# Kernel tuning notes

Measured on AMD Instinct MI355X. Metric: run time of the kernel, lower is better.

Reference implementation:

```python
import jax, jax.numpy as jnp
import numpy as np

B, T = 1024, 128
F_DIM, Z_DIM, TXT_DIM, H = 1024, 256, 768, 8
EPS = 1e-5


def layer_norm(x, g, b):
    mu = jnp.mean(x, axis=-1, keepdims=True)
    var = jnp.var(x, axis=-1, keepdims=True)
    return (x - mu) * jax.lax.rsqrt(var + EPS) * g + b


def setup_inputs() -> dict:
    key = jax.random.key(0)
    ks = jax.random.split(key, 16)
    s = lambda fi, fo: 1.0 / np.sqrt(fi)  # rough init scale
    inp = {
        "x": jax.random.normal(ks[0], (B, F_DIM), jnp.float32),
        "z": jax.random.normal(ks[1], (B, Z_DIM), jnp.float32),
        "text_feat": jax.random.normal(ks[2], (B, T, TXT_DIM), jnp.float32),
        "attention": jnp.ones((B, T), jnp.int32),
        # FiLM
        "Wg": jax.random.normal(ks[3], (F_DIM, Z_DIM), jnp.float32) * s(Z_DIM, F_DIM),
        "bg": jnp.zeros((F_DIM,), jnp.float32),
        "Wb": jax.random.normal(ks[4], (F_DIM, Z_DIM), jnp.float32) * s(Z_DIM, F_DIM),
        "bb": jnp.zeros((F_DIM,), jnp.float32),
        # Linear block (linear -> LayerNorm)
        "Wl": jax.random.normal(ks[5], (F_DIM, F_DIM), jnp.float32) * s(F_DIM, F_DIM),
        "bl": jnp.zeros((F_DIM,), jnp.float32),
        "ln1_g": jnp.ones((F_DIM,), jnp.float32),
        "ln1_b": jnp.zeros((F_DIM,), jnp.float32),
        # cross attention projections
        "Wq": jax.random.normal(ks[6], (F_DIM, F_DIM), jnp.float32) * s(F_DIM, F_DIM),
        "bq": jnp.zeros((F_DIM,), jnp.float32),
        "Wk": jax.random.normal(ks[7], (F_DIM, TXT_DIM), jnp.float32) * s(TXT_DIM, F_DIM),
        "bk": jnp.zeros((F_DIM,), jnp.float32),
        "Wv": jax.random.normal(ks[8], (F_DIM, TXT_DIM), jnp.float32) * s(TXT_DIM, F_DIM),
        "bv": jnp.zeros((F_DIM,), jnp.float32),
        "Wo": jax.random.normal(ks[9], (F_DIM, F_DIM), jnp.float32) * s(F_DIM, F_DIM),
        "bo": jnp.zeros((F_DIM,), jnp.float32),
        # post-attention LayerNorm
        "ln2_g": jnp.ones((F_DIM,), jnp.float32),
        "ln2_b": jnp.zeros((F_DIM,), jnp.float32),
    }
    return inp


def reference(x, z, text_feat, attention, Wg, bg, Wb, bb, Wl, bl, ln1_g, ln1_b,
              Wq, bq, Wk, bk, Wv, bv, Wo, bo, ln2_g, ln2_b):
    d = F_DIM // H
    # FiLM params from condition z
    gamma = z @ Wg.T + bg            # [B, F]
    beta = z @ Wb.T + bb             # [B, F]
    # Linear block: linear -> LayerNorm (dropout p=0, identity activation)
    out = layer_norm(x @ Wl.T + bl, ln1_g, ln1_b)
    out = out * (1.0 + gamma) + beta  # FiLM modulation
    # single-query multi-head cross attention
    q = (out @ Wq.T + bq).reshape(B, H, d)                 # [B, H, d] (query len 1)
    k = (text_feat @ Wk.T + bk).reshape(B, T, H, d)         # [B, T, H, d]
    v = (text_feat @ Wv.T + bv).reshape(B, T, H, d)
    scores = jnp.einsum("bhd,bthd->bht", q, k) / jnp.sqrt(jnp.float32(d))  # [B, H, T]
    mask = (attention[:, None, :] != 0)                     # [B, 1, T]
    scores = jnp.where(mask, scores, -jnp.inf)
    attn = jax.nn.softmax(scores, axis=-1)                  # [B, H, T]
    ctx = jnp.einsum("bht,bthd->bhd", attn, v).reshape(B, F_DIM)
    attn_out = ctx @ Wo.T + bo
    out = out + layer_norm(attn_out, ln2_g, ln2_b)
    return jax.nn.gelu(out, approximate=False)
```

## Files before the change

kernel.cpp:

```cpp
#include <hip/hip_runtime.h>

#define EPS 1e-5f

typedef __bf16 bf16x8 __attribute__((ext_vector_type(8)));
typedef float f32x4 __attribute__((ext_vector_type(4)));
typedef ushort ushort8 __attribute__((ext_vector_type(8)));

static __device__ __forceinline__ ushort f2bf(float x) {
    union { float f; unsigned u; } v; v.f = x;
    unsigned r = v.u + 0x7fffu + ((v.u >> 16) & 1u);
    return (ushort)(r >> 16);
}
static __device__ __forceinline__ float bf2f(ushort u) {
    union { unsigned u32; float f; } v; v.u32 = (unsigned)u << 16;
    return v.f;
}

__global__ __launch_bounds__(256)
void gemm_nt_mfma(const float* __restrict__ A, int lda, int Aoffz,
                  const ushort* __restrict__ W, int ldw, int Woffz,
                  float* __restrict__ C, int ldc, int Coffz,
                  const float* __restrict__ bias, int boffz,
                  float scale, int K)
{
    const int z = blockIdx.z;
    A += (size_t)z * Aoffz;
    W += (size_t)z * Woffz;
    C += (size_t)z * Coffz;
    const int bm = blockIdx.y * 64, bn = blockIdx.x * 64;

    __shared__ ushort As[64][72];
    __shared__ ushort Bs[64][72];

    const int tid  = threadIdx.x;
    const int lane = tid & 63, wv = tid >> 6;
    const int wm = (wv >> 1) * 32, wn = (wv & 1) * 32;

    const int srow = tid >> 2;
    const int scol = (tid & 3) * 16;
    const float*  Agp = A + (size_t)(bm + srow) * lda + scol;
    const ushort* Wgp = W + (size_t)(bn + srow) * ldw + scol;

    const int fr = lane & 15, fk = (lane >> 4) * 8;

    f32x4 acc[2][2] = {};

    for (int kt = 0; kt < K; kt += 64) {
        f32x4 a0 = *(const f32x4*)(Agp + kt + 0);
        f32x4 a1 = *(const f32x4*)(Agp + kt + 4);
        f32x4 a2 = *(const f32x4*)(Agp + kt + 8);
        f32x4 a3 = *(const f32x4*)(Agp + kt + 12);
        ushort8 b0 = *(const ushort8*)(Wgp + kt);
        ushort8 b1 = *(const ushort8*)(Wgp + kt + 8);

        ushort8 u0, u1;
        u0[0]=f2bf(a0[0]); u0[1]=f2bf(a0[1]); u0[2]=f2bf(a0[2]); u0[3]=f2bf(a0[3]);
        u0[4]=f2bf(a1[0]); u0[5]=f2bf(a1[1]); u0[6]=f2bf(a1[2]); u0[7]=f2bf(a1[3]);
        u1[0]=f2bf(a2[0]); u1[1]=f2bf(a2[1]); u1[2]=f2bf(a2[2]); u1[3]=f2bf(a2[3]);
        u1[4]=f2bf(a3[0]); u1[5]=f2bf(a3[1]); u1[6]=f2bf(a3[2]); u1[7]=f2bf(a3[3]);

        *(ushort8*)&As[srow][scol]     = u0;
        *(ushort8*)&As[srow][scol + 8] = u1;
        *(ushort8*)&Bs[srow][scol]     = b0;
        *(ushort8*)&Bs[srow][scol + 8] = b1;
        __syncthreads();

        #pragma unroll
        for (int ks = 0; ks < 64; ks += 32) {
            bf16x8 af0 = *(const bf16x8*)&As[wm + fr][ks + fk];
            bf16x8 af1 = *(const bf16x8*)&As[wm + 16 + fr][ks + fk];
            bf16x8 bf0 = *(const bf16x8*)&Bs[wn + fr][ks + fk];
            bf16x8 bf1 = *(const bf16x8*)&Bs[wn + 16 + fr][ks + fk];
            acc[0][0] = __builtin_amdgcn_mfma_f32_16x16x32_bf16(af0, bf0, acc[0][0], 0, 0, 0);
            acc[0][1] = __builtin_amdgcn_mfma_f32_16x16x32_bf16(af0, bf1, acc[0][1], 0, 0, 0);
            acc[1][0] = __builtin_amdgcn_mfma_f32_16x16x32_bf16(af1, bf0, acc[1][0], 0, 0, 0);
            acc[1][1] = __builtin_amdgcn_mfma_f32_16x16x32_bf16(af1, bf1, acc[1][1], 0, 0, 0);
        }
        __syncthreads();
    }

    const int rbase = (lane >> 4) * 4;
    #pragma unroll
    for (int mi = 0; mi < 2; ++mi) {
        #pragma unroll
        for (int ni = 0; ni < 2; ++ni) {
            const int col = bn + wn + ni * 16 + fr;
            const float bvv = bias ? (bias + (size_t)z * boffz)[col] : 0.f;
            #pragma unroll
            for (int r = 0; r < 4; ++r) {
                const int row = bm + wm + mi * 16 + rbase + r;
                C[(size_t)row * ldc + col] = acc[mi][ni][r] * scale + bvv;
            }
        }
    }
}

__global__ __launch_bounds__(256)
void cvt_all(const float* __restrict__ Wl, const float* __restrict__ Wq,
             const float* __restrict__ Wo, const float* __restrict__ Wv,
             const float* __restrict__ Wg, const float* __restrict__ Wb,
             const float* __restrict__ bg, const float* __restrict__ bb,
             ushort* __restrict__ WlB, ushort* __restrict__ WqB,
             ushort* __restrict__ WoB, ushort* __restrict__ WvB,
             ushort* __restrict__ WgbB, float* __restrict__ bgb)
{
    int gid = blockIdx.x * 256 + threadIdx.x;
    if (gid < 512) {
        f32x4 v = (gid < 256) ? *(const f32x4*)(bg + gid * 4)
                              : *(const f32x4*)(bb + (gid - 256) * 4);
        *(f32x4*)(bgb + gid * 4) = v;
    }
    const float* src; ushort* dst; int off;
    if      (gid <  262144) { src = Wl; dst = WlB;           off = gid;          }
    else if (gid <  524288) { src = Wq; dst = WqB;           off = gid - 262144; }
    else if (gid <  786432) { src = Wo; dst = WoB;           off = gid - 524288; }
    else if (gid <  983040) { src = Wv; dst = WvB;           off = gid - 786432; }
    else if (gid < 1048576) { src = Wg; dst = WgbB;          off = gid - 983040; }
    else if (gid < 1114112) { src = Wb; dst = WgbB + 262144; off = gid - 1048576;}
    else return;
    f32x4 v = *(const f32x4*)(src + (size_t)off * 4);
    ushort4 o;
    o.x = f2bf(v[0]); o.y = f2bf(v[1]); o.z = f2bf(v[2]); o.w = f2bf(v[3]);
    *(ushort4*)(dst + (size_t)off * 4) = o;
}

__global__ __launch_bounds__(256)
void transpose_wk(const float* __restrict__ Wk, ushort* __restrict__ WkT)
{
    __shared__ ushort s[32][33];
    const int h  = blockIdx.z;
    const int c0 = blockIdx.x * 32, d0 = blockIdx.y * 32;
    const int tx = threadIdx.x & 31, ty = threadIdx.x >> 5;
    #pragma unroll
    for (int i = 0; i < 4; ++i) {
        int d = d0 + ty + i * 8;
        s[ty + i * 8][tx] = f2bf(Wk[(size_t)(h * 128 + d) * 768 + c0 + tx]);
    }
    __syncthreads();
    #pragma unroll
    for (int i = 0; i < 4; ++i) {
        int c = c0 + ty + i * 8;
        WkT[((size_t)h * 768 + c) * 128 + d0 + tx] = s[tx][ty + i * 8];
    }
}

__device__ inline void block_reduce2(float& a, float& b, float* sred)
{
    #pragma unroll
    for (int off = 32; off; off >>= 1) {
        a += __shfl_xor(a, off);
        b += __shfl_xor(b, off);
    }
    int w = threadIdx.x >> 6, lane = threadIdx.x & 63;
    if (lane == 0) { sred[w * 2] = a; sred[w * 2 + 1] = b; }
    __syncthreads();
    a = sred[0] + sred[2] + sred[4] + sred[6];
    b = sred[1] + sred[3] + sred[5] + sred[7];
}

__global__ __launch_bounds__(256)
void rowops1(const float* __restrict__ h1, const float* __restrict__ gb,
             const float* __restrict__ g, const float* __restrict__ bta,
             float* __restrict__ out)
{
    __shared__ float sred[8];
    int b = blockIdx.x, tid = threadIdx.x;
    const float4 v = ((const float4*)(h1 + (size_t)b * 1024))[tid];
    float s  = v.x + v.y + v.z + v.w;
    float ss = v.x * v.x + v.y * v.y + v.z * v.z + v.w * v.w;
    block_reduce2(s, ss, sred);
    float mu  = s * (1.f / 1024.f);
    float var = ss * (1.f / 1024.f) - mu * mu;
    float rs  = rsqrtf(var + EPS);
    float4 gv = ((const float4*)g)[tid];
    float4 bv = ((const float4*)bta)[tid];
    float4 ga = ((const float4*)(gb + (size_t)b * 2048))[tid];
    float4 be = ((const float4*)(gb + (size_t)b * 2048 + 1024))[tid];
    float4 o;
    o.x = ((v.x - mu) * rs * gv.x + bv.x) * (1.f + ga.x) + be.x;
    o.y = ((v.y - mu) * rs * gv.y + bv.y) * (1.f + ga.y) + be.y;
    o.z = ((v.z - mu) * rs * gv.z + bv.z) * (1.f + ga.z) + be.z;
    o.w = ((v.w - mu) * rs * gv.w + bv.w) * (1.f + ga.w) + be.w;
    ((float4*)(out + (size_t)b * 1024))[tid] = o;
}

__global__ __launch_bounds__(256)
void rowops2(const float* __restrict__ outp, const float* __restrict__ ao,
             const float* __restrict__ g, const float* __restrict__ bta,
             float* __restrict__ dst)
{
    __shared__ float sred[8];
    int b = blockIdx.x, tid = threadIdx.x;
    const float4 v = ((const float4*)(ao + (size_t)b * 1024))[tid];
    float s  = v.x + v.y + v.z + v.w;
    float ss = v.x * v.x + v.y * v.y + v.z * v.z + v.w * v.w;
    block_reduce2(s, ss, sred);
    float mu  = s * (1.f / 1024.f);
    float var = ss * (1.f / 1024.f) - mu * mu;
    float rs  = rsqrtf(var + EPS);
    float4 gv = ((const float4*)g)[tid];
    float4 bv = ((const float4*)bta)[tid];
    float4 ov = ((const float4*)(outp + (size_t)b * 1024))[tid];
    float y0 = ov.x + ((v.x - mu) * rs * gv.x + bv.x);
    float y1 = ov.y + ((v.y - mu) * rs * gv.y + bv.y);
    float y2 = ov.z + ((v.z - mu) * rs * gv.z + bv.z);
    float y3 = ov.w + ((v.w - mu) * rs * gv.w + bv.w);
    float4 o;
    o.x = 0.5f * y0 * (1.f + erff(y0 * 0.70710678118654752f));
    o.y = 0.5f * y1 * (1.f + erff(y1 * 0.70710678118654752f));
    o.z = 0.5f * y2 * (1.f + erff(y2 * 0.70710678118654752f));
    o.w = 0.5f * y3 * (1.f + erff(y3 * 0.70710678118654752f));
    ((float4*)(dst + (size_t)b * 1024))[tid] = o;
}

__global__ __launch_bounds__(256)
void attn_fused(const float* __restrict__ tf, const float* __restrict__ qt,
                const int* __restrict__ att, float* __restrict__ ctxtf)
{
    const int b = blockIdx.x;
    const int tid = threadIdx.x, lane = tid & 63, wv = tid >> 6;

    __shared__ ushort qtS[16][776];
    __shared__ ushort TF[32][776];
    __shared__ float s_sc[8][32];
    __shared__ float ps[8][32];

    const float* tfb = tf + (size_t)b * 98304;
    const float* qtb = qt + (size_t)b * 6144;

    {
        const int r  = tid >> 5;
        const int c0 = (tid & 31) * 24;
        #pragma unroll
        for (int j = 0; j < 6; ++j) {
            f32x4 v = *(const f32x4*)&qtb[r * 768 + c0 + 4 * j];
            ushort4 o;
            o.x = f2bf(v[0]); o.y = f2bf(v[1]); o.z = f2bf(v[2]); o.w = f2bf(v[3]);
            *(ushort4*)&qtS[r][c0 + 4 * j] = o;
        }
        const ushort4 z4 = {0, 0, 0, 0};
        #pragma unroll
        for (int j = 0; j < 6; ++j)
            *(ushort4*)&qtS[8 + r][c0 + 4 * j] = z4;
    }

    float acc[2][3][4] = {};
    float mrun = -INFINITY, srun = 0.f;
    const int fr = lane & 15, fko = (lane >> 4) * 8;
    const int hloc = lane >> 5, tl = lane & 31;
    const int h_own = 2 * wv + hloc;
    const int h0 = 2 * wv;

    for (int s = 0; s < 4; ++s) {
        __syncthreads();
        {
            const int r  = tid >> 3;
            const int c0 = (tid & 7) * 96;
            const float* srcr = tfb + (size_t)(s * 32 + r) * 768 + c0;
            #pragma unroll
            for (int j = 0; j < 24; ++j) {
                f32x4 v = *(const f32x4*)(srcr + 4 * j);
                ushort4 o;
                o.x = f2bf(v[0]); o.y = f2bf(v[1]); o.z = f2bf(v[2]); o.w = f2bf(v[3]);
                *(ushort4*)&TF[r][c0 + 4 * j] = o;
            }
        }
        __syncthreads();
        if (wv < 2) {
            f32x4 sacc = {0.f, 0.f, 0.f, 0.f};
            #pragma unroll
            for (int ks = 0; ks < 768; ks += 32) {
                bf16x8 aq = *(const bf16x8*)&qtS[fr][ks + fko];
                bf16x8 bt = *(const bf16x8*)&TF[wv * 16 + fr][ks + fko];
                sacc = __builtin_amdgcn_mfma_f32_16x16x32_bf16(aq, bt, sacc, 0, 0, 0);
            }
            if (lane < 32) {
                const int hbase = (lane >> 4) * 4;
                #pragma unroll
                for (int r = 0; r < 4; ++r)
                    s_sc[hbase + r][wv * 16 + (lane & 15)] = sacc[r];
            }
        }
        __syncthreads();
        {
            const int mask = att[b * 128 + s * 32 + tl];
            float sv = mask ? s_sc[h_own][tl] : -INFINITY;
            float mx = sv;
            mx = fmaxf(mx, __shfl_xor(mx, 16));
            mx = fmaxf(mx, __shfl_xor(mx, 8));
            mx = fmaxf(mx, __shfl_xor(mx, 4));
            mx = fmaxf(mx, __shfl_xor(mx, 2));
            mx = fmaxf(mx, __shfl_xor(mx, 1));
            float mnew = fmaxf(mrun, mx);
            float p = mask ? __expf(sv - mnew) : 0.f;
            float f = (mnew == -INFINITY) ? 1.f : __expf(mrun - mnew);
            float psum = p;
            psum += __shfl_xor(psum, 16);
            psum += __shfl_xor(psum, 8);
            psum += __shfl_xor(psum, 4);
            psum += __shfl_xor(psum, 2);
            psum += __shfl_xor(psum, 1);
            srun = srun * f + psum;
            mrun = mnew;
            ps[h_own][tl] = p;
            const float f0 = __shfl(f, 0);
            const float f1 = __shfl(f, 32);
            #pragma unroll
            for (int k = 0; k < 3; ++k)
                #pragma unroll
                for (int e = 0; e < 4; ++e) {
                    acc[0][k][e] *= f0;
                    acc[1][k][e] *= f1;
                }
        }
        {
            #pragma unroll 8
            for (int t = 0; t < 32; ++t) {
                const float p0 = ps[h0][t];
                const float p1 = ps[h0 + 1][t];
                #pragma unroll
                for (int k = 0; k < 3; ++k) {
                    ushort4 u = *(const ushort4*)&TF[t][4 * lane + 256 * k];
                    float x0 = bf2f(u.x), x1 = bf2f(u.y), x2 = bf2f(u.z), x3 = bf2f(u.w);
                    acc[0][k][0] += p0 * x0; acc[0][k][1] += p0 * x1;
                    acc[0][k][2] += p0 * x2; acc[0][k][3] += p0 * x3;
                    acc[1][k][0] += p1 * x0; acc[1][k][1] += p1 * x1;
                    acc[1][k][2] += p1 * x2; acc[1][k][3] += p1 * x3;
                }
            }
        }
    }

    const float sum0 = __shfl(srun, 0);
    const float sum1 = __shfl(srun, 32);
    const float i0 = 1.f / sum0, i1 = 1.f / sum1;
    #pragma unroll
    for (int k = 0; k < 3; ++k) {
        f32x4 o0, o1;
        #pragma unroll
        for (int e = 0; e < 4; ++e) {
            o0[e] = acc[0][k][e] * i0;
            o1[e] = acc[1][k][e] * i1;
        }
        *(f32x4*)&ctxtf[(size_t)b * 6144 + (size_t)h0 * 768 + 4 * lane + 256 * k] = o0;
        *(f32x4*)&ctxtf[(size_t)b * 6144 + (size_t)(h0 + 1) * 768 + 4 * lane + 256 * k] = o1;
    }
}

extern "C" void kernel_launch(void* const* d_in, const int* in_sizes, int n_in,
                              void* d_out, int out_size, void* d_ws, size_t ws_size,
                              hipStream_t stream)
{
    const float* x    = (const float*)d_in[0];
    const float* zc   = (const float*)d_in[1];
    const float* tf   = (const float*)d_in[2];
    const int*   att  = (const int*)d_in[3];
    const float* Wg   = (const float*)d_in[4];
    const float* bg   = (const float*)d_in[5];
    const float* Wb   = (const float*)d_in[6];
    const float* bb   = (const float*)d_in[7];
    const float* Wl   = (const float*)d_in[8];
    const float* bl   = (const float*)d_in[9];
    const float* ln1g = (const float*)d_in[10];
    const float* ln1b = (const float*)d_in[11];
    const float* Wq   = (const float*)d_in[12];
    const float* bq   = (const float*)d_in[13];
    const float* Wk   = (const float*)d_in[14];
    const float* Wv   = (const float*)d_in[16];
    const float* bv   = (const float*)d_in[17];
    const float* Wo   = (const float*)d_in[18];
    const float* bo   = (const float*)d_in[19];
    const float* ln2g = (const float*)d_in[20];
    const float* ln2b = (const float*)d_in[21];

    float* ws = (float*)d_ws;
    const size_t M1 = 1u << 20;
    float* OUT   = ws;
    float* H1    = ws + 1 * M1;
    float* GB    = ws + 2 * M1;
    float* Q     = ws + 4 * M1;
    float* QT    = ws + 5 * M1;
    float* CTXTF = ws + 11 * M1;
    float* AO    = ws + 17 * M1;
    float* bgb   = ws + 18 * M1;
    float* CTX   = H1;

    ushort* wb16 = (ushort*)(ws + 19 * M1);
    ushort* WlB  = wb16;
    ushort* WqB  = wb16 + 1 * M1;
    ushort* WoB  = wb16 + 2 * M1;
    ushort* WvB  = wb16 + 3 * M1;
    ushort* WgbB = wb16 + 3 * M1 + 786432;
    ushort* WkT  = wb16 + 3 * M1 + 786432 + 524288;

    dim3 blk(256);

    cvt_all<<<dim3(4352), blk, 0, stream>>>(Wl, Wq, Wo, Wv, Wg, Wb, bg, bb,
                                            WlB, WqB, WoB, WvB, WgbB, bgb);
    transpose_wk<<<dim3(24, 4, 8), blk, 0, stream>>>(Wk, WkT);

    gemm_nt_mfma<<<dim3(16, 16, 1), blk, 0, stream>>>(x, 1024, 0, WlB, 1024, 0,
        H1, 1024, 0, bl, 0, 1.f, 1024);
    gemm_nt_mfma<<<dim3(32, 16, 1), blk, 0, stream>>>(zc, 256, 0, WgbB, 256, 0,
        GB, 2048, 0, bgb, 0, 1.f, 256);
    rowops1<<<dim3(1024), blk, 0, stream>>>(H1, GB, ln1g, ln1b, OUT);
    gemm_nt_mfma<<<dim3(16, 16, 1), blk, 0, stream>>>(OUT, 1024, 0, WqB, 1024, 0,
        Q, 1024, 0, bq, 0, 1.f, 1024);
    gemm_nt_mfma<<<dim3(12, 16, 8), blk, 0, stream>>>(Q, 1024, 128, WkT, 128, 98304,
        QT, 6144, 768, nullptr, 0, 0.08838834764831845f, 128);
    attn_fused<<<dim3(1024), blk, 0, stream>>>(tf, QT, att, CTXTF);
    gemm_nt_mfma<<<dim3(2, 16, 8), blk, 0, stream>>>(CTXTF, 6144, 768, WvB, 768, 98304,
        CTX, 1024, 128, bv, 128, 1.f, 768);
    gemm_nt_mfma<<<dim3(16, 16, 1), blk, 0, stream>>>(CTX, 1024, 0, WoB, 1024, 0,
        AO, 1024, 0, bo, 0, 1.f, 1024);
    rowops2<<<dim3(1024), blk, 0, stream>>>(OUT, AO, ln2g, ln2b, (float*)d_out);
}
```

Measured before the change: 709.0 us.

## Store intermediates in bf16 and prefetch next K tile in GEMM

```diff
diff --git a/kernel.cpp b/kernel.cpp
--- a/kernel.cpp
+++ b/kernel.cpp
@@ -16,17 +16,17 @@
     return v.f;
 }
 
-__global__ __launch_bounds__(256)
-void gemm_nt_mfma(const float* __restrict__ A, int lda, int Aoffz,
-                  const ushort* __restrict__ W, int ldw, int Woffz,
-                  float* __restrict__ C, int ldc, int Coffz,
-                  const float* __restrict__ bias, int boffz,
-                  float scale, int K)
+template<int OB>
+__global__ __launch_bounds__(256)
+void gemm_bb(const ushort* __restrict__ A, int lda, int Aoffz,
+             const ushort* __restrict__ W, int ldw, int Woffz,
+             void* __restrict__ Cv, int ldc, int Coffz,
+             const float* __restrict__ bias, int boffz,
+             float scale, int K)
 {
     const int z = blockIdx.z;
     A += (size_t)z * Aoffz;
     W += (size_t)z * Woffz;
-    C += (size_t)z * Coffz;
     const int bm = blockIdx.y * 64, bn = blockIdx.x * 64;
 
     __shared__ ushort As[64][72];
@@ -38,33 +38,30 @@
 
     const int srow = tid >> 2;
     const int scol = (tid & 3) * 16;
-    const float*  Agp = A + (size_t)(bm + srow) * lda + scol;
+    const ushort* Agp = A + (size_t)(bm + srow) * lda + scol;
     const ushort* Wgp = W + (size_t)(bn + srow) * ldw + scol;
 
     const int fr = lane & 15, fk = (lane >> 4) * 8;
 
     f32x4 acc[2][2] = {};
 
+    ushort8 a0 = *(const ushort8*)(Agp);
+    ushort8 a1 = *(const ushort8*)(Agp + 8);
+    ushort8 b0 = *(const ushort8*)(Wgp);
+    ushort8 b1 = *(const ushort8*)(Wgp + 8);
+
     for (int kt = 0; kt < K; kt += 64) {
-        f32x4 a0 = *(const f32x4*)(Agp + kt + 0);
-        f32x4 a1 = *(const f32x4*)(Agp + kt + 4);
-        f32x4 a2 = *(const f32x4*)(Agp + kt + 8);
-        f32x4 a3 = *(const f32x4*)(Agp + kt + 12);
-        ushort8 b0 = *(const ushort8*)(Wgp + kt);
-        ushort8 b1 = *(const ushort8*)(Wgp + kt + 8);
-
-        ushort8 u0, u1;
-        u0[0]=f2bf(a0[0]); u0[1]=f2bf(a0[1]); u0[2]=f2bf(a0[2]); u0[3]=f2bf(a0[3]);
-        u0[4]=f2bf(a1[0]); u0[5]=f2bf(a1[1]); u0[6]=f2bf(a1[2]); u0[7]=f2bf(a1[3]);
-        u1[0]=f2bf(a2[0]); u1[1]=f2bf(a2[1]); u1[2]=f2bf(a2[2]); u1[3]=f2bf(a2[3]);
-        u1[4]=f2bf(a3[0]); u1[5]=f2bf(a3[1]); u1[6]=f2bf(a3[2]); u1[7]=f2bf(a3[3]);
-
-        *(ushort8*)&As[srow][scol]     = u0;
-        *(ushort8*)&As[srow][scol + 8] = u1;
+        *(ushort8*)&As[srow][scol]     = a0;
+        *(ushort8*)&As[srow][scol + 8] = a1;
         *(ushort8*)&Bs[srow][scol]     = b0;
         *(ushort8*)&Bs[srow][scol + 8] = b1;
         __syncthreads();
-
+        if (kt + 64 < K) {
+            a0 = *(const ushort8*)(Agp + kt + 64);
+            a1 = *(const ushort8*)(Agp + kt + 64 + 8);
+            b0 = *(const ushort8*)(Wgp + kt + 64);
+            b1 = *(const ushort8*)(Wgp + kt + 64 + 8);
+        }
         #pragma unroll
         for (int ks = 0; ks < 64; ks += 32) {
             bf16x8 af0 = *(const bf16x8*)&As[wm + fr][ks + fk];
@@ -89,7 +86,12 @@
             #pragma unroll
             for (int r = 0; r < 4; ++r) {
                 const int row = bm + wm + mi * 16 + rbase + r;
-                C[(size_t)row * ldc + col] = acc[mi][ni][r] * scale + bvv;
+                const float val = acc[mi][ni][r] * scale + bvv;
+                if (OB) {
+                    ((ushort*)Cv)[(size_t)z * Coffz + (size_t)row * ldc + col] = f2bf(val);
+                } else {
+                    ((float*)Cv)[(size_t)z * Coffz + (size_t)row * ldc + col] = val;
+                }
             }
         }
     }
@@ -99,10 +101,12 @@
 void cvt_all(const float* __restrict__ Wl, const float* __restrict__ Wq,
              const float* __restrict__ Wo, const float* __restrict__ Wv,
              const float* __restrict__ Wg, const float* __restrict__ Wb,
+             const float* __restrict__ x,  const float* __restrict__ zc,
              const float* __restrict__ bg, const float* __restrict__ bb,
              ushort* __restrict__ WlB, ushort* __restrict__ WqB,
              ushort* __restrict__ WoB, ushort* __restrict__ WvB,
-             ushort* __restrict__ WgbB, float* __restrict__ bgb)
+             ushort* __restrict__ WgbB, ushort* __restrict__ xB,
+             ushort* __restrict__ zB, float* __restrict__ bgb)
 {
     int gid = blockIdx.x * 256 + threadIdx.x;
     if (gid < 512) {
@@ -117,6 +121,8 @@
     else if (gid <  983040) { src = Wv; dst = WvB;           off = gid - 786432; }
     else if (gid < 1048576) { src = Wg; dst = WgbB;          off = gid - 983040; }
     else if (gid < 1114112) { src = Wb; dst = WgbB + 262144; off = gid - 1048576;}
+    else if (gid < 1376256) { src = x;  dst = xB;            off = gid - 1114112;}
+    else if (gid < 1441792) { src = zc; dst = zB;            off = gid - 1376256;}
     else return;
     f32x4 v = *(const f32x4*)(src + (size_t)off * 4);
     ushort4 o;
@@ -161,7 +167,7 @@
 __global__ __launch_bounds__(256)
 void rowops1(const float* __restrict__ h1, const float* __restrict__ gb,
              const float* __restrict__ g, const float* __restrict__ bta,
-             float* __restrict__ out)
+             ushort* __restrict__ outb)
 {
     __shared__ float sred[8];
     int b = blockIdx.x, tid = threadIdx.x;
@@ -176,16 +182,16 @@
     float4 bv = ((const float4*)bta)[tid];
     float4 ga = ((const float4*)(gb + (size_t)b * 2048))[tid];
     float4 be = ((const float4*)(gb + (size_t)b * 2048 + 1024))[tid];
-    float4 o;
-    o.x = ((v.x - mu) * rs * gv.x + bv.x) * (1.f + ga.x) + be.x;
-    o.y = ((v.y - mu) * rs * gv.y + bv.y) * (1.f + ga.y) + be.y;
-    o.z = ((v.z - mu) * rs * gv.z + bv.z) * (1.f + ga.z) + be.z;
-    o.w = ((v.w - mu) * rs * gv.w + bv.w) * (1.f + ga.w) + be.w;
-    ((float4*)(out + (size_t)b * 1024))[tid] = o;
-}
-
-__global__ __launch_bounds__(256)
-void rowops2(const float* __restrict__ outp, const float* __restrict__ ao,
+    ushort4 o;
+    o.x = f2bf(((v.x - mu) * rs * gv.x + bv.x) * (1.f + ga.x) + be.x);
+    o.y = f2bf(((v.y - mu) * rs * gv.y + bv.y) * (1.f + ga.y) + be.y);
+    o.z = f2bf(((v.z - mu) * rs * gv.z + bv.z) * (1.f + ga.z) + be.z);
+    o.w = f2bf(((v.w - mu) * rs * gv.w + bv.w) * (1.f + ga.w) + be.w);
+    ((ushort4*)(outb + (size_t)b * 1024))[tid] = o;
+}
+
+__global__ __launch_bounds__(256)
+void rowops2(const ushort* __restrict__ outb, const float* __restrict__ ao,
              const float* __restrict__ g, const float* __restrict__ bta,
              float* __restrict__ dst)
 {
@@ -200,11 +206,11 @@
     float rs  = rsqrtf(var + EPS);
     float4 gv = ((const float4*)g)[tid];
     float4 bv = ((const float4*)bta)[tid];
-    float4 ov = ((const float4*)(outp + (size_t)b * 1024))[tid];
-    float y0 = ov.x + ((v.x - mu) * rs * gv.x + bv.x);
-    float y1 = ov.y + ((v.y - mu) * rs * gv.y + bv.y);
-    float y2 = ov.z + ((v.z - mu) * rs * gv.z + bv.z);
-    float y3 = ov.w + ((v.w - mu) * rs * gv.w + bv.w);
+    ushort4 ou = ((const ushort4*)(outb + (size_t)b * 1024))[tid];
+    float y0 = bf2f(ou.x) + ((v.x - mu) * rs * gv.x + bv.x);
+    float y1 = bf2f(ou.y) + ((v.y - mu) * rs * gv.y + bv.y);
+    float y2 = bf2f(ou.z) + ((v.z - mu) * rs * gv.z + bv.z);
+    float y3 = bf2f(ou.w) + ((v.w - mu) * rs * gv.w + bv.w);
     float4 o;
     o.x = 0.5f * y0 * (1.f + erff(y0 * 0.70710678118654752f));
     o.y = 0.5f * y1 * (1.f + erff(y1 * 0.70710678118654752f));
@@ -214,8 +220,8 @@
 }
 
 __global__ __launch_bounds__(256)
-void attn_fused(const float* __restrict__ tf, const float* __restrict__ qt,
-                const int* __restrict__ att, float* __restrict__ ctxtf)
+void attn_fused(const float* __restrict__ tf, const ushort* __restrict__ qt,
+                const int* __restrict__ att, ushort* __restrict__ ctxtf)
 {
     const int b = blockIdx.x;
     const int tid = threadIdx.x, lane = tid & 63, wv = tid >> 6;
@@ -225,23 +231,19 @@
     __shared__ float s_sc[8][32];
     __shared__ float ps[8][32];
 
-    const float* tfb = tf + (size_t)b * 98304;
-    const float* qtb = qt + (size_t)b * 6144;
+    const float*  tfb = tf + (size_t)b * 98304;
+    const ushort* qtb = qt + (size_t)b * 6144;
 
     {
         const int r  = tid >> 5;
         const int c0 = (tid & 31) * 24;
         #pragma unroll
-        for (int j = 0; j < 6; ++j) {
-            f32x4 v = *(const f32x4*)&qtb[r * 768 + c0 + 4 * j];
-            ushort4 o;
-            o.x = f2bf(v[0]); o.y = f2bf(v[1]); o.z = f2bf(v[2]); o.w = f2bf(v[3]);
-            *(ushort4*)&qtS[r][c0 + 4 * j] = o;
-        }
-        const ushort4 z4 = {0, 0, 0, 0};
+        for (int j = 0; j < 3; ++j)
+            *(ushort8*)&qtS[r][c0 + 8 * j] = *(const ushort8*)&qtb[r * 768 + c0 + 8 * j];
+        const ushort8 z8 = {0,0,0,0,0,0,0,0};
         #pragma unroll
-        for (int j = 0; j < 6; ++j)
-            *(ushort4*)&qtS[8 + r][c0 + 4 * j] = z4;
+        for (int j = 0; j < 3; ++j)
+            *(ushort8*)&qtS[8 + r][c0 + 8 * j] = z8;
     }
 
     float acc[2][3][4] = {};
@@ -336,14 +338,13 @@
     const float i0 = 1.f / sum0, i1 = 1.f / sum1;
     #pragma unroll
     for (int k = 0; k < 3; ++k) {
-        f32x4 o0, o1;
-        #pragma unroll
-        for (int e = 0; e < 4; ++e) {
-            o0[e] = acc[0][k][e] * i0;
-            o1[e] = acc[1][k][e] * i1;
-        }
-        *(f32x4*)&ctxtf[(size_t)b * 6144 + (size_t)h0 * 768 + 4 * lane + 256 * k] = o0;
-        *(f32x4*)&ctxtf[(size_t)b * 6144 + (size_t)(h0 + 1) * 768 + 4 * lane + 256 * k] = o1;
+        ushort4 o0, o1;
+        o0.x = f2bf(acc[0][k][0] * i0); o0.y = f2bf(acc[0][k][1] * i0);
+        o0.z = f2bf(acc[0][k][2] * i0); o0.w = f2bf(acc[0][k][3] * i0);
+        o1.x = f2bf(acc[1][k][0] * i1); o1.y = f2bf(acc[1][k][1] * i1);
+        o1.z = f2bf(acc[1][k][2] * i1); o1.w = f2bf(acc[1][k][3] * i1);
+        *(ushort4*)&ctxtf[(size_t)b * 6144 + (size_t)h0 * 768 + 4 * lane + 256 * k] = o0;
+        *(ushort4*)&ctxtf[(size_t)b * 6144 + (size_t)(h0 + 1) * 768 + 4 * lane + 256 * k] = o1;
     }
 }
 
@@ -375,43 +376,45 @@
 
     float* ws = (float*)d_ws;
     const size_t M1 = 1u << 20;
-    float* OUT   = ws;
-    float* H1    = ws + 1 * M1;
-    float* GB    = ws + 2 * M1;
-    float* Q     = ws + 4 * M1;
-    float* QT    = ws + 5 * M1;
-    float* CTXTF = ws + 11 * M1;
-    float* AO    = ws + 17 * M1;
-    float* bgb   = ws + 18 * M1;
-    float* CTX   = H1;
-
-    ushort* wb16 = (ushort*)(ws + 19 * M1);
-    ushort* WlB  = wb16;
-    ushort* WqB  = wb16 + 1 * M1;
-    ushort* WoB  = wb16 + 2 * M1;
-    ushort* WvB  = wb16 + 3 * M1;
-    ushort* WgbB = wb16 + 3 * M1 + 786432;
-    ushort* WkT  = wb16 + 3 * M1 + 786432 + 524288;
+    float* H1  = ws;
+    float* GB  = ws + 1 * M1;
+    float* AO  = ws + 3 * M1;
+    float* bgb = ws + 4 * M1;
+
+    ushort* u = (ushort*)(ws + 5 * M1);
+    ushort* WlB  = u;
+    ushort* WqB  = u + 1 * M1;
+    ushort* WoB  = u + 2 * M1;
+    ushort* WvB  = u + 3 * M1;
+    ushort* WgbB = u + 3 * M1 + 786432;
+    ushort* WkT  = u + 3 * M1 + 1310720;
+    ushort* xB   = u + 5 * M1;
+    ushort* zB   = u + 6 * M1;
+    ushort* OUTB = u + 6 * M1 + 262144;
+    ushort* Q    = u + 7 * M1 + 262144;
+    ushort* QT   = u + 8 * M1 + 262144;
+    ushort* CTXB = u + 14 * M1 + 262144;
+    ushort* CTX  = u + 20 * M1 + 262144;
 
     dim3 blk(256);
 
-    cvt_all<<<dim3(4352), blk, 0, stream>>>(Wl, Wq, Wo, Wv, Wg, Wb, bg, bb,
-                                            WlB, WqB, WoB, WvB, WgbB, bgb);
+    cvt_all<<<dim3(5632), blk, 0, stream>>>(Wl, Wq, Wo, Wv, Wg, Wb, x, zc, bg, bb,
+                                            WlB, WqB, WoB, WvB, WgbB, xB, zB, bgb);
     transpose_wk<<<dim3(24, 4, 8), blk, 0, stream>>>(Wk, WkT);
 
-    gemm_nt_mfma<<<dim3(16, 16, 1), blk, 0, stream>>>(x, 1024, 0, WlB, 1024, 0,
-        H1, 1024, 0, bl, 0, 1.f, 1024);
-    gemm_nt_mfma<<<dim3(32, 16, 1), blk, 0, stream>>>(zc, 256, 0, WgbB, 256, 0,
-        GB, 2048, 0, bgb, 0, 1.f, 256);
-    rowops1<<<dim3(1024), blk, 0, stream>>>(H1, GB, ln1g, ln1b, OUT);
-    gemm_nt_mfma<<<dim3(16, 16, 1), blk, 0, stream>>>(OUT, 1024, 0, WqB, 1024, 0,
-        Q, 1024, 0, bq, 0, 1.f, 1024);
-    gemm_nt_mfma<<<dim3(12, 16, 8), blk, 0, stream>>>(Q, 1024, 128, WkT, 128, 98304,
-        QT, 6144, 768, nullptr, 0, 0.08838834764831845f, 128);
-    attn_fused<<<dim3(1024), blk, 0, stream>>>(tf, QT, att, CTXTF);
-    gemm_nt_mfma<<<dim3(2, 16, 8), blk, 0, stream>>>(CTXTF, 6144, 768, WvB, 768, 98304,
-        CTX, 1024, 128, bv, 128, 1.f, 768);
-    gemm_nt_mfma<<<dim3(16, 16, 1), blk, 0, stream>>>(CTX, 1024, 0, WoB, 1024, 0,
-        AO, 1024, 0, bo, 0, 1.f, 1024);
-    rowops2<<<dim3(1024), blk, 0, stream>>>(OUT, AO, ln2g, ln2b, (float*)d_out);
-}
+    gemm_bb<0><<<dim3(16, 16, 1), blk, 0, stream>>>(xB, 1024, 0, WlB, 1024, 0,
+        (void*)H1, 1024, 0, bl, 0, 1.f, 1024);
+    gemm_bb<0><<<dim3(32, 16, 1), blk, 0, stream>>>(zB, 256, 0, WgbB, 256, 0,
+        (void*)GB, 2048, 0, bgb, 0, 1.f, 256);
+    rowops1<<<dim3(1024), blk, 0, stream>>>(H1, GB, ln1g, ln1b, OUTB);
+    gemm_bb<1><<<dim3(16, 16, 1), blk, 0, stream>>>(OUTB, 1024, 0, WqB, 1024, 0,
+        (void*)Q, 1024, 0, bq, 0, 1.f, 1024);
+    gemm_bb<1><<<dim3(12, 16, 8), blk, 0, stream>>>(Q, 1024, 128, WkT, 128, 98304,
+        (void*)QT, 6144, 768, nullptr, 0, 0.08838834764831845f, 128);
+    attn_fused<<<dim3(1024), blk, 0, stream>>>(tf, QT, att, CTXB);
+    gemm_bb<1><<<dim3(2, 16, 8), blk, 0, stream>>>(CTXB, 6144, 768, WvB, 768, 98304,
+        (void*)CTX, 1024, 128, bv, 128, 1.f, 768);
+    gemm_bb<0><<<dim3(16, 16, 1), blk, 0, stream>>>(CTX, 1024, 0, WoB, 1024, 0,
+        (void*)AO, 1024, 0, bo, 0, 1.f, 1024);
+    rowops2<<<dim3(1024), blk, 0, stream>>>(OUTB, AO, ln2g, ln2b, (float*)d_out);
+}
```

Result: faster. 673.8 us (-5.0%).
